# Kernel optimization log

Measured on AMD Instinct MI355X. Metric: run time of the kernel, lower is better.

The kernel has to match this reference:

```python
import jax, jax.numpy as jnp
import numpy as np

NEG_INF = -1e30  # stand-in for -inf, avoids NaN under masked rows edge cases


def setup_inputs() -> dict:
    key = jax.random.key(0)
    ks = jax.random.split(key, 6)
    H, N, F_IN, HD, F_OUT = 8, 4096, 512, 64, 512
    X = jax.random.normal(ks[0], (H, N, F_IN), dtype=jnp.float32)
    mask = jax.random.randint(ks[1], (H, N, N), 0, 2, dtype=jnp.int32)
    s = 1.0 / np.sqrt(F_IN)
    W_Q = jax.random.normal(ks[2], (H, HD, F_IN), dtype=jnp.float32) * s
    W_K = jax.random.normal(ks[3], (H, HD, F_IN), dtype=jnp.float32) * s
    W_V = jax.random.normal(ks[4], (H, HD, F_IN), dtype=jnp.float32) * s
    W_O = jax.random.normal(ks[5], (F_OUT, H * HD), dtype=jnp.float32) * (1.0 / np.sqrt(H * HD))
    return {"X": X, "mask": mask, "W_Q": W_Q, "W_K": W_K, "W_V": W_V, "W_O": W_O}


def reference(X, mask, W_Q, W_K, W_V, W_O):
    # X: [H, N, F_in]; W_{Q,K,V}: [H, head_dim, F_in] (torch Linear layout: [out,in])
    Q = jnp.einsum('hnf,hdf->hnd', X, W_Q)
    K = jnp.einsum('hnf,hdf->hnd', X, W_K)
    V = jnp.einsum('hnf,hdf->hnd', X, W_V)
    head_dim = K.shape[-1]
    E = jnp.einsum('hnd,hmd->hnm', Q, K) / jnp.sqrt(jnp.float32(head_dim))  # [H,N,N]
    E = jnp.where(mask == 0, jnp.float32(NEG_INF), E)
    A = jax.nn.softmax(E, axis=-1)
    Hout = jnp.einsum('hnm,hmd->hnd', A, V)  # [H, N, head_dim]
    # concat heads along feature dim -> [N, H*head_dim]
    Hcat = jnp.transpose(Hout, (1, 0, 2)).reshape(Hout.shape[1], -1)
    # dropout is identity in eval mode
    return Hcat @ W_O.T  # [N, fan_out]
```

## Files before the change

### kernel.cpp

```cpp
#include <hip/hip_runtime.h>

typedef __bf16 bf16x8 __attribute__((ext_vector_type(8)));
typedef float f32x4 __attribute__((ext_vector_type(4)));

#define MFMA(a, b, c) __builtin_amdgcn_mfma_f32_16x16x32_bf16((a), (b), (c), 0, 0, 0)
#define GLOAD_LDS(g, l) __builtin_amdgcn_global_load_lds( \
    (const __attribute__((address_space(1))) void*)(g),   \
    (__attribute__((address_space(3))) void*)(l), 16, 0, 0)

constexpr int HEADS = 8, SEQ = 4096, FIN = 512, HD = 64, FOUT = 512;
constexpr float QSCALE = 0.18033688011112042f;

__device__ inline bf16x8 cvt8(const float* __restrict__ p) {
    f32x4 a = *(const f32x4*)p;
    f32x4 b = *(const f32x4*)(p + 4);
    bf16x8 r;
    r[0] = (__bf16)a[0]; r[1] = (__bf16)a[1]; r[2] = (__bf16)a[2]; r[3] = (__bf16)a[3];
    r[4] = (__bf16)b[0]; r[5] = (__bf16)b[1]; r[6] = (__bf16)b[2]; r[7] = (__bf16)b[3];
    return r;
}

__global__ __launch_bounds__(256) void qkv_kernel(
    const float* __restrict__ X, const float* __restrict__ Wq,
    const float* __restrict__ Wk, const float* __restrict__ Wv,
    __bf16* __restrict__ Q, __bf16* __restrict__ K, __bf16* __restrict__ Vt)
{
    const int h = blockIdx.y;
    const int tid = threadIdx.x;
    const int w = tid >> 6, lane = tid & 63;
    const int quad = lane >> 4, l16 = lane & 15;
    const int m = blockIdx.x * 64 + w * 16 + l16;

    const float* xrow = X + ((size_t)h * SEQ + m) * FIN + quad * 8;
    const float* wqh = Wq + (size_t)h * HD * FIN + quad * 8;
    const float* wkh = Wk + (size_t)h * HD * FIN + quad * 8;
    const float* wvh = Wv + (size_t)h * HD * FIN + quad * 8;

    const f32x4 vzero = {0.f, 0.f, 0.f, 0.f};
    f32x4 accQ[4], accK[4], accV[4];
#pragma unroll
    for (int t = 0; t < 4; ++t) { accQ[t] = vzero; accK[t] = vzero; accV[t] = vzero; }

    for (int f0 = 0; f0 < FIN; f0 += 32) {
        bf16x8 a = cvt8(xrow + f0);
#pragma unroll
        for (int t = 0; t < 4; ++t) {
            const int wrow = (t * 16 + l16) * FIN + f0;
            bf16x8 bq = cvt8(wqh + wrow);
            bf16x8 bk = cvt8(wkh + wrow);
            bf16x8 bv = cvt8(wvh + wrow);
            accQ[t] = MFMA(a, bq, accQ[t]);
            accK[t] = MFMA(a, bk, accK[t]);
            accV[t] = MFMA(a, bv, accV[t]);
        }
    }

    const int row0 = blockIdx.x * 64 + w * 16 + quad * 4;
#pragma unroll
    for (int t = 0; t < 4; ++t) {
        const int d = t * 16 + l16;
#pragma unroll
        for (int r = 0; r < 4; ++r) {
            const int n = row0 + r;
            Q[((size_t)h * SEQ + n) * HD + d] = (__bf16)(accQ[t][r] * QSCALE);
            K[((size_t)h * SEQ + n) * HD + d] = (__bf16)accK[t][r];
            Vt[((size_t)h * HD + d) * SEQ + n] = (__bf16)accV[t][r];
        }
    }
}

__global__ __launch_bounds__(256) void attn_kernel(
    const __bf16* __restrict__ Q, const __bf16* __restrict__ K,
    const __bf16* __restrict__ Vt, const int* __restrict__ mask,
    __bf16* __restrict__ Hcat)
{
    __shared__ __align__(16) unsigned char lds[32768 + 4 * 2304];
    __bf16* ldsK = (__bf16*)lds;
    __bf16* ldsV = (__bf16*)(lds + 8192);
    int*    ldsM = (int*)(lds + 16384);

    const int h = blockIdx.y;
    const int tid = threadIdx.x;
    const int w = tid >> 6, lane = tid & 63;
    const int quad = lane >> 4, l16 = lane & 15;
    const int q0b = blockIdx.x * 64;
    const int q0 = q0b + w * 16;

    __bf16* pl = (__bf16*)(lds + 32768) + w * 1152;

    const __bf16* Qh = Q + (size_t)h * SEQ * HD;
    const __bf16* Kh = K + (size_t)h * SEQ * HD;
    const __bf16* Vh = Vt + (size_t)h * HD * SEQ;
    const int* mh = mask + (size_t)h * SEQ * SEQ;

    bf16x8 qa0 = *(const bf16x8*)(Qh + (size_t)(q0 + l16) * HD + quad * 8);
    bf16x8 qa1 = *(const bf16x8*)(Qh + (size_t)(q0 + l16) * HD + 32 + quad * 8);

    const f32x4 vzero = {0.f, 0.f, 0.f, 0.f};
    f32x4 O[4];
    float lsum[4] = {0.f, 0.f, 0.f, 0.f};
#pragma unroll
    for (int t = 0; t < 4; ++t) O[t] = vzero;

    for (int n0 = 0; n0 < SEQ; n0 += 64) {
#pragma unroll
        for (int c = 0; c < 2; ++c) {
            const int s = (c * 4 + w) * 64 + lane;
            const int row = s >> 3;
            const int cq = (s & 7) ^ (row & 7);
            GLOAD_LDS(Kh + (size_t)(n0 + row) * HD + cq * 8,
                      (unsigned char*)ldsK + (c * 4 + w) * 1024);
            GLOAD_LDS(Vh + (size_t)row * SEQ + n0 + cq * 8,
                      (unsigned char*)ldsV + (c * 4 + w) * 1024);
        }
#pragma unroll
        for (int c = 0; c < 4; ++c) {
            const int s = (c * 4 + w) * 64 + lane;
            const int row = s >> 4;
            const int ch = s & 15;
            GLOAD_LDS(mh + (size_t)(q0b + row) * SEQ + n0 + ch * 4,
                      (unsigned char*)ldsM + (c * 4 + w) * 1024);
        }
        __syncthreads();

        f32x4 S[4];
#pragma unroll
        for (int t = 0; t < 4; ++t) {
            const int r16 = t * 16 + l16;
            bf16x8 kb0 = *(const bf16x8*)(ldsK + r16 * 64 + ((quad ^ (r16 & 7)) * 8));
            bf16x8 kb1 = *(const bf16x8*)(ldsK + r16 * 64 + (((quad + 4) ^ (r16 & 7)) * 8));
            S[t] = MFMA(qa0, kb0, vzero);
            S[t] = MFMA(qa1, kb1, S[t]);
        }

#pragma unroll
        for (int t = 0; t < 4; ++t) {
#pragma unroll
            for (int r = 0; r < 4; ++r) {
                const int mk = ldsM[(w * 16 + quad * 4 + r) * 64 + t * 16 + l16];
                float p = __builtin_amdgcn_exp2f(S[t][r]);
                p = mk ? p : 0.f;
                lsum[r] += p;
                pl[(quad * 4 + r) * 72 + t * 16 + l16] = (__bf16)p;
            }
        }

        bf16x8 pa0 = *(const bf16x8*)(pl + l16 * 72 + quad * 8);
        bf16x8 pa1 = *(const bf16x8*)(pl + l16 * 72 + 32 + quad * 8);
#pragma unroll
        for (int t = 0; t < 4; ++t) {
            const int d = t * 16 + l16;
            bf16x8 vb0 = *(const bf16x8*)(ldsV + d * 64 + ((quad ^ (d & 7)) * 8));
            bf16x8 vb1 = *(const bf16x8*)(ldsV + d * 64 + (((quad + 4) ^ (d & 7)) * 8));
            O[t] = MFMA(pa0, vb0, O[t]);
            O[t] = MFMA(pa1, vb1, O[t]);
        }
        __syncthreads();
    }

#pragma unroll
    for (int r = 0; r < 4; ++r) {
#pragma unroll
        for (int off = 1; off < 16; off <<= 1)
            lsum[r] += __shfl_xor(lsum[r], off, 64);
    }

#pragma unroll
    for (int r = 0; r < 4; ++r) {
        const float inv = lsum[r] > 0.f ? 1.0f / lsum[r] : 0.f;
        const int n = q0 + quad * 4 + r;
#pragma unroll
        for (int t = 0; t < 4; ++t)
            Hcat[(size_t)n * FOUT + h * HD + t * 16 + l16] = (__bf16)(O[t][r] * inv);
    }
}

__global__ __launch_bounds__(256) void out_kernel(
    const __bf16* __restrict__ Hcat, const float* __restrict__ Wo,
    float* __restrict__ out)
{
    const int tid = threadIdx.x;
    const int w = tid >> 6, lane = tid & 63;
    const int quad = lane >> 4, l16 = lane & 15;
    const int n0 = blockIdx.x * 64 + w * 16;
    const int o0 = blockIdx.y * 64;

    const f32x4 vzero = {0.f, 0.f, 0.f, 0.f};
    f32x4 acc[4];
#pragma unroll
    for (int t = 0; t < 4; ++t) acc[t] = vzero;

    for (int k0 = 0; k0 < FOUT; k0 += 32) {
        bf16x8 a = *(const bf16x8*)(Hcat + (size_t)(n0 + l16) * FOUT + k0 + quad * 8);
#pragma unroll
        for (int t = 0; t < 4; ++t) {
            bf16x8 b = cvt8(Wo + (size_t)(o0 + t * 16 + l16) * FOUT + k0 + quad * 8);
            acc[t] = MFMA(a, b, acc[t]);
        }
    }
#pragma unroll
    for (int t = 0; t < 4; ++t)
#pragma unroll
        for (int r = 0; r < 4; ++r)
            out[(size_t)(n0 + quad * 4 + r) * FOUT + o0 + t * 16 + l16] = acc[t][r];
}

extern "C" void kernel_launch(void* const* d_in, const int* in_sizes, int n_in,
                              void* d_out, int out_size, void* d_ws, size_t ws_size,
                              hipStream_t stream) {
    const float* X    = (const float*)d_in[0];
    const int*   mask = (const int*)d_in[1];
    const float* Wq   = (const float*)d_in[2];
    const float* Wk   = (const float*)d_in[3];
    const float* Wv   = (const float*)d_in[4];
    const float* Wo   = (const float*)d_in[5];
    float* out = (float*)d_out;

    __bf16* Q    = (__bf16*)d_ws;
    __bf16* K    = Q + (size_t)HEADS * SEQ * HD;
    __bf16* Vt   = K + (size_t)HEADS * SEQ * HD;
    __bf16* Hcat = Vt + (size_t)HEADS * HD * SEQ;

    qkv_kernel<<<dim3(SEQ / 64, HEADS), 256, 0, stream>>>(X, Wq, Wk, Wv, Q, K, Vt);
    attn_kernel<<<dim3(SEQ / 64, HEADS), 256, 0, stream>>>(Q, K, Vt, mask, Hcat);
    out_kernel<<<dim3(SEQ / 64, FOUT / 64), 256, 0, stream>>>(Hcat, Wo, out);
}
```

Before: 911.1 us.

## Pack int32 mask into bitmask in a pre-pass and load bits per block

A new pack kernel streams the int32 mask once and writes a 1-bit-per-element bitmask using wave ballots. The attention kernel then preloads its 64 rows of packed mask into LDS up front instead of streaming int32 mask tiles every iteration. Mask traffic in the attention loop drops, but the mask still has to be read in full by the extra kernel and LDS use grows, which may reduce occupancy.

```diff
diff --git a/kernel.cpp b/kernel.cpp
--- a/kernel.cpp
+++ b/kernel.cpp
@@ -20,6 +20,25 @@
     return r;
 }
 
+__global__ __launch_bounds__(256) void pack_kernel(
+    const int* __restrict__ m, unsigned long long* __restrict__ pm)
+{
+    const int lane = threadIdx.x & 63;
+    const int wid = (int)((blockIdx.x * 256 + threadIdx.x) >> 6);
+    const int nw = (int)((gridDim.x * 256) >> 6);
+    const size_t total = (size_t)HEADS * SEQ * SEQ;
+    for (size_t base = (size_t)wid * 512; base < total; base += (size_t)nw * 512) {
+        int v[8];
+#pragma unroll
+        for (int j = 0; j < 8; ++j) v[j] = m[base + (size_t)j * 64 + lane];
+#pragma unroll
+        for (int j = 0; j < 8; ++j) {
+            unsigned long long b = __ballot(v[j] != 0);
+            if (lane == j) pm[base / 64 + j] = b;
+        }
+    }
+}
+
 __global__ __launch_bounds__(256) void qkv_kernel(
     const float* __restrict__ X, const float* __restrict__ Wq,
     const float* __restrict__ Wk, const float* __restrict__ Wv,
@@ -71,13 +90,13 @@
 
 __global__ __launch_bounds__(256) void attn_kernel(
     const __bf16* __restrict__ Q, const __bf16* __restrict__ K,
-    const __bf16* __restrict__ Vt, const int* __restrict__ mask,
+    const __bf16* __restrict__ Vt, const unsigned long long* __restrict__ pm,
     __bf16* __restrict__ Hcat)
 {
-    __shared__ __align__(16) unsigned char lds[32768 + 4 * 2304];
-    __bf16* ldsK = (__bf16*)lds;
-    __bf16* ldsV = (__bf16*)(lds + 8192);
-    int*    ldsM = (int*)(lds + 16384);
+    __shared__ __align__(16) unsigned char lds[49152 + 4 * 2304];
+    unsigned int* ldsPM = (unsigned int*)lds;
+    __bf16* ldsK = (__bf16*)(lds + 32768);
+    __bf16* ldsV = (__bf16*)(lds + 40960);
 
     const int h = blockIdx.y;
     const int tid = threadIdx.x;
@@ -86,12 +105,20 @@
     const int q0b = blockIdx.x * 64;
     const int q0 = q0b + w * 16;
 
-    __bf16* pl = (__bf16*)(lds + 32768) + w * 1152;
+    __bf16* pl = (__bf16*)(lds + 49152) + w * 1152;
 
     const __bf16* Qh = Q + (size_t)h * SEQ * HD;
     const __bf16* Kh = K + (size_t)h * SEQ * HD;
     const __bf16* Vh = Vt + (size_t)h * HD * SEQ;
-    const int* mh = mask + (size_t)h * SEQ * SEQ;
+
+    {
+        const unsigned char* pmb = (const unsigned char*)(pm + ((size_t)h * SEQ + q0b) * (SEQ / 64));
+#pragma unroll
+        for (int c = 0; c < 8; ++c) {
+            const int chunk = c * 256 + w * 64 + lane;
+            GLOAD_LDS(pmb + (size_t)chunk * 16, lds + (c * 256 + w * 64) * 16);
+        }
+    }
 
     bf16x8 qa0 = *(const bf16x8*)(Qh + (size_t)(q0 + l16) * HD + quad * 8);
     bf16x8 qa1 = *(const bf16x8*)(Qh + (size_t)(q0 + l16) * HD + 32 + quad * 8);
@@ -113,14 +140,6 @@
             GLOAD_LDS(Vh + (size_t)row * SEQ + n0 + cq * 8,
                       (unsigned char*)ldsV + (c * 4 + w) * 1024);
         }
-#pragma unroll
-        for (int c = 0; c < 4; ++c) {
-            const int s = (c * 4 + w) * 64 + lane;
-            const int row = s >> 4;
-            const int ch = s & 15;
-            GLOAD_LDS(mh + (size_t)(q0b + row) * SEQ + n0 + ch * 4,
-                      (unsigned char*)ldsM + (c * 4 + w) * 1024);
-        }
         __syncthreads();
 
         f32x4 S[4];
@@ -134,12 +153,16 @@
         }
 
 #pragma unroll
-        for (int t = 0; t < 4; ++t) {
-#pragma unroll
-            for (int r = 0; r < 4; ++r) {
-                const int mk = ldsM[(w * 16 + quad * 4 + r) * 64 + t * 16 + l16];
+        for (int r = 0; r < 4; ++r) {
+            const unsigned int* pmrow = ldsPM + (w * 16 + quad * 4 + r) * 128 + (n0 >> 5);
+            const unsigned int mlo = pmrow[0];
+            const unsigned int mhi = pmrow[1];
+#pragma unroll
+            for (int t = 0; t < 4; ++t) {
+                const unsigned int word = (t < 2) ? mlo : mhi;
+                const unsigned int bit = (word >> ((t & 1) * 16 + l16)) & 1u;
                 float p = __builtin_amdgcn_exp2f(S[t][r]);
-                p = mk ? p : 0.f;
+                p = bit ? p : 0.f;
                 lsum[r] += p;
                 pl[(quad * 4 + r) * 72 + t * 16 + l16] = (__bf16)p;
             }
@@ -220,8 +243,11 @@
     __bf16* K    = Q + (size_t)HEADS * SEQ * HD;
     __bf16* Vt   = K + (size_t)HEADS * SEQ * HD;
     __bf16* Hcat = Vt + (size_t)HEADS * HD * SEQ;
-
+    unsigned long long* pm =
+        (unsigned long long*)(Hcat + (size_t)SEQ * FOUT);
+
+    pack_kernel<<<2048, 256, 0, stream>>>(mask, pm);
     qkv_kernel<<<dim3(SEQ / 64, HEADS), 256, 0, stream>>>(X, Wq, Wk, Wv, Q, K, Vt);
-    attn_kernel<<<dim3(SEQ / 64, HEADS), 256, 0, stream>>>(Q, K, Vt, mask, Hcat);
+    attn_kernel<<<dim3(SEQ / 64, HEADS), 256, 0, stream>>>(Q, K, Vt, pm, Hcat);
     out_kernel<<<dim3(SEQ / 64, FOUT / 64), 256, 0, stream>>>(Hcat, Wo, out);
 }
```

After: 958.2 us. +5.2%, slower.

## Double-buffer attention K/V/mask tiles and compute S transposed for vectorized mask reads

Applied to the files above, without the earlier changes.

Splits the attention kernel's LDS into two buffers so the next K, V and mask tile is prefetched with global_load_lds while the current tile is computed, dropping one barrier per iteration. It also swaps the MFMA operands to compute S transposed, so each lane reads four contiguous mask ints as one vector load and writes packed 64-bit P values. The row sum becomes a single per-lane accumulator reduced with a few shuffles. The XOR swizzle on K/V in LDS is removed, which may bring back bank conflicts, and LDS use grows to about 74KB, which may limit occupancy.

```diff
diff --git a/kernel.cpp b/kernel.cpp
--- a/kernel.cpp
+++ b/kernel.cpp
@@ -2,6 +2,7 @@
 
 typedef __bf16 bf16x8 __attribute__((ext_vector_type(8)));
 typedef float f32x4 __attribute__((ext_vector_type(4)));
+typedef int i32x4 __attribute__((ext_vector_type(4)));
 
 #define MFMA(a, b, c) __builtin_amdgcn_mfma_f32_16x16x32_bf16((a), (b), (c), 0, 0, 0)
 #define GLOAD_LDS(g, l) __builtin_amdgcn_global_load_lds( \
@@ -74,10 +75,7 @@
     const __bf16* __restrict__ Vt, const int* __restrict__ mask,
     __bf16* __restrict__ Hcat)
 {
-    __shared__ __align__(16) unsigned char lds[32768 + 4 * 2304];
-    __bf16* ldsK = (__bf16*)lds;
-    __bf16* ldsV = (__bf16*)(lds + 8192);
-    int*    ldsM = (int*)(lds + 16384);
+    __shared__ __align__(16) unsigned char lds[65536 + 4 * 2304];
 
     const int h = blockIdx.y;
     const int tid = threadIdx.x;
@@ -86,92 +84,107 @@
     const int q0b = blockIdx.x * 64;
     const int q0 = q0b + w * 16;
 
-    __bf16* pl = (__bf16*)(lds + 32768) + w * 1152;
+    __bf16* PT = (__bf16*)(lds + 65536) + w * 1152;
 
     const __bf16* Qh = Q + (size_t)h * SEQ * HD;
     const __bf16* Kh = K + (size_t)h * SEQ * HD;
     const __bf16* Vh = Vt + (size_t)h * HD * SEQ;
     const int* mh = mask + (size_t)h * SEQ * SEQ;
 
+    const int sKV = w * 64 + lane;
+    const int sM  = w * 64 + lane;
+
+    auto stage = [&](int n0, int b) {
+        unsigned char* bK = lds + 32768 + b * 8192;
+        unsigned char* bV = lds + 49152 + b * 8192;
+        unsigned char* bM = lds + b * 16384;
+        const __bf16* Kn = Kh + (size_t)n0 * HD;
+#pragma unroll
+        for (int c = 0; c < 2; ++c) {
+            const int s = c * 256 + sKV;
+            GLOAD_LDS(Kn + s * 8, bK + s * 16);
+            GLOAD_LDS(Vh + (size_t)(s >> 3) * SEQ + n0 + (s & 7) * 8, bV + s * 16);
+        }
+#pragma unroll
+        for (int c = 0; c < 4; ++c) {
+            const int s = c * 256 + sM;
+            GLOAD_LDS(mh + (size_t)(q0b + (s >> 4)) * SEQ + n0 + (s & 15) * 4, bM + s * 16);
+        }
+    };
+
     bf16x8 qa0 = *(const bf16x8*)(Qh + (size_t)(q0 + l16) * HD + quad * 8);
     bf16x8 qa1 = *(const bf16x8*)(Qh + (size_t)(q0 + l16) * HD + 32 + quad * 8);
 
     const f32x4 vzero = {0.f, 0.f, 0.f, 0.f};
     f32x4 O[4];
-    float lsum[4] = {0.f, 0.f, 0.f, 0.f};
+    float lsum = 0.f;
 #pragma unroll
     for (int t = 0; t < 4; ++t) O[t] = vzero;
 
-    for (int n0 = 0; n0 < SEQ; n0 += 64) {
-#pragma unroll
-        for (int c = 0; c < 2; ++c) {
-            const int s = (c * 4 + w) * 64 + lane;
-            const int row = s >> 3;
-            const int cq = (s & 7) ^ (row & 7);
-            GLOAD_LDS(Kh + (size_t)(n0 + row) * HD + cq * 8,
-                      (unsigned char*)ldsK + (c * 4 + w) * 1024);
-            GLOAD_LDS(Vh + (size_t)row * SEQ + n0 + cq * 8,
-                      (unsigned char*)ldsV + (c * 4 + w) * 1024);
-        }
-#pragma unroll
-        for (int c = 0; c < 4; ++c) {
-            const int s = (c * 4 + w) * 64 + lane;
-            const int row = s >> 4;
-            const int ch = s & 15;
-            GLOAD_LDS(mh + (size_t)(q0b + row) * SEQ + n0 + ch * 4,
-                      (unsigned char*)ldsM + (c * 4 + w) * 1024);
-        }
-        __syncthreads();
-
-        f32x4 S[4];
-#pragma unroll
-        for (int t = 0; t < 4; ++t) {
-            const int r16 = t * 16 + l16;
-            bf16x8 kb0 = *(const bf16x8*)(ldsK + r16 * 64 + ((quad ^ (r16 & 7)) * 8));
-            bf16x8 kb1 = *(const bf16x8*)(ldsK + r16 * 64 + (((quad + 4) ^ (r16 & 7)) * 8));
-            S[t] = MFMA(qa0, kb0, vzero);
-            S[t] = MFMA(qa1, kb1, S[t]);
-        }
-
-#pragma unroll
-        for (int t = 0; t < 4; ++t) {
+    stage(0, 0);
+    __syncthreads();
+
+    for (int i = 0; i < SEQ / 64; ++i) {
+        const int n0 = i * 64;
+        const int cur = i & 1;
+        if (i + 1 < SEQ / 64) stage(n0 + 64, cur ^ 1);
+
+        const __bf16* cK = (const __bf16*)(lds + 32768 + cur * 8192);
+        const __bf16* cV = (const __bf16*)(lds + 49152 + cur * 8192);
+        const unsigned char* cM = lds + cur * 16384;
+
+        f32x4 St[4];
+#pragma unroll
+        for (int t = 0; t < 4; ++t) {
+            const int kr = t * 16 + l16;
+            bf16x8 kb0 = *(const bf16x8*)(cK + kr * 64 + quad * 8);
+            bf16x8 kb1 = *(const bf16x8*)(cK + kr * 64 + 32 + quad * 8);
+            St[t] = MFMA(kb0, qa0, vzero);
+            St[t] = MFMA(kb1, qa1, St[t]);
+        }
+
+#pragma unroll
+        for (int t = 0; t < 4; ++t) {
+            i32x4 mv = *(const i32x4*)(cM + ((w * 16 + l16) * 64 + t * 16 + quad * 4) * 4);
+            union { unsigned long long u; __bf16 hh[4]; } pk;
 #pragma unroll
             for (int r = 0; r < 4; ++r) {
-                const int mk = ldsM[(w * 16 + quad * 4 + r) * 64 + t * 16 + l16];
-                float p = __builtin_amdgcn_exp2f(S[t][r]);
-                p = mk ? p : 0.f;
-                lsum[r] += p;
-                pl[(quad * 4 + r) * 72 + t * 16 + l16] = (__bf16)p;
+                float p = __builtin_amdgcn_exp2f(St[t][r]);
+                p = mv[r] ? p : 0.f;
+                lsum += p;
+                pk.hh[r] = (__bf16)p;
             }
-        }
-
-        bf16x8 pa0 = *(const bf16x8*)(pl + l16 * 72 + quad * 8);
-        bf16x8 pa1 = *(const bf16x8*)(pl + l16 * 72 + 32 + quad * 8);
-#pragma unroll
-        for (int t = 0; t < 4; ++t) {
-            const int d = t * 16 + l16;
-            bf16x8 vb0 = *(const bf16x8*)(ldsV + d * 64 + ((quad ^ (d & 7)) * 8));
-            bf16x8 vb1 = *(const bf16x8*)(ldsV + d * 64 + (((quad + 4) ^ (d & 7)) * 8));
+            *(unsigned long long*)(PT + l16 * 72 + t * 16 + quad * 4) = pk.u;
+        }
+
+        bf16x8 pa0 = *(const bf16x8*)(PT + l16 * 72 + quad * 8);
+        bf16x8 pa1 = *(const bf16x8*)(PT + l16 * 72 + 32 + quad * 8);
+#pragma unroll
+        for (int t = 0; t < 4; ++t) {
+            const int dr = t * 16 + l16;
+            bf16x8 vb0 = *(const bf16x8*)(cV + dr * 64 + quad * 8);
+            bf16x8 vb1 = *(const bf16x8*)(cV + dr * 64 + 32 + quad * 8);
             O[t] = MFMA(pa0, vb0, O[t]);
             O[t] = MFMA(pa1, vb1, O[t]);
         }
         __syncthreads();
     }
 
+    lsum += __shfl_xor(lsum, 16, 64);
+    lsum += __shfl_xor(lsum, 32, 64);
+    float inv[4];
 #pragma unroll
     for (int r = 0; r < 4; ++r) {
-#pragma unroll
-        for (int off = 1; off < 16; off <<= 1)
-            lsum[r] += __shfl_xor(lsum[r], off, 64);
+        float Lr = __shfl(lsum, quad * 4 + r, 64);
+        inv[r] = Lr > 0.f ? 1.0f / Lr : 0.f;
     }
 
 #pragma unroll
     for (int r = 0; r < 4; ++r) {
-        const float inv = lsum[r] > 0.f ? 1.0f / lsum[r] : 0.f;
         const int n = q0 + quad * 4 + r;
 #pragma unroll
         for (int t = 0; t < 4; ++t)
-            Hcat[(size_t)n * FOUT + h * HD + t * 16 + l16] = (__bf16)(O[t][r] * inv);
+            Hcat[(size_t)n * FOUT + h * HD + t * 16 + l16] = (__bf16)(O[t][r] * inv[r]);
     }
 }
 
```

Measured after the change: 911.8 us. Within noise of the previous version (+0.1%).
